# Optimization experiments

Measured on AMD Instinct MI355X. Metric: run time of the kernel, lower is better.

## Reference

```python
import jax, jax.numpy as jnp
import numpy as np

EPS = 1e-7  # tf.keras.backend.epsilon()

def setup_inputs() -> dict:
    key = jax.random.key(0)
    k1, k2, k3, k4 = jax.random.split(key, 4)
    B, S, D = 8, 2048, 768
    scale = 1.0 / np.sqrt(D)
    return {
        "x1": jax.random.normal(k1, (B, S, D), dtype=jnp.float32),
        "x2": jax.random.normal(k2, (B, S, D), dtype=jnp.float32),
        "Wq": jax.random.normal(k3, (D, D), dtype=jnp.float32) * scale,
        "bq": jnp.zeros((D,), dtype=jnp.float32),
        "Wk": jax.random.normal(k4, (D, D), dtype=jnp.float32) * scale,
        "bk": jnp.zeros((D,), dtype=jnp.float32),
    }

def reference(x1, x2, Wq, bq, Wk, bk):
    # q: [B,S1,D], k: [B,S2,D]
    q = jnp.einsum('bsd,de->bse', x1, Wq) + bq
    k = jnp.einsum('btd,de->bte', x2, Wk) + bk
    qk = jnp.einsum('bsd,btd->bst', q, k)          # [B,S1,S2]
    w = jnp.exp(jnp.tanh(qk))
    w = w / (jnp.sum(w, axis=1, keepdims=True) + EPS)  # normalize over S1
    return jnp.sum(w * qk, axis=1)                 # [B,S2]
```

## Files before the change

### kernel.cpp

```cpp
#include <hip/hip_runtime.h>
#include <hip/hip_bf16.h>

typedef __bf16 bf16_t;
typedef __bf16 bf16x8 __attribute__((ext_vector_type(8)));
typedef __bf16 bf16x4 __attribute__((ext_vector_type(4)));
typedef float  f32x4  __attribute__((ext_vector_type(4)));

#define D_DIM 768
#define S_DIM 2048
#define B_DIM 8
#define M_TOT (B_DIM * S_DIM)
#define BK 32
#define LDS_PAD 40

__global__ __launch_bounds__(256)
void transpose_weights(const float* __restrict__ Wq, const float* __restrict__ Wk,
                       bf16_t* __restrict__ Wqt, bf16_t* __restrict__ Wkt) {
    __shared__ float tile[32][33];
    const float* W  = blockIdx.z ? Wk  : Wq;
    bf16_t*      Wt = blockIdx.z ? Wkt : Wqt;
    int tx = threadIdx.x & 31, ty = threadIdx.x >> 5;
    int bx = blockIdx.x, by = blockIdx.y;
#pragma unroll
    for (int i = 0; i < 4; i++) {
        int k = bx * 32 + ty + i * 8;
        int n = by * 32 + tx;
        tile[ty + i * 8][tx] = W[k * D_DIM + n];
    }
    __syncthreads();
#pragma unroll
    for (int i = 0; i < 4; i++) {
        int n = by * 32 + ty + i * 8;
        int k = bx * 32 + tx;
        Wt[n * D_DIM + k] = (bf16_t)tile[tx][ty + i * 8];
    }
}

__global__ __launch_bounds__(256)
void proj_gemm(const float* __restrict__ X, const bf16_t* __restrict__ Wt,
               const float* __restrict__ bias, bf16_t* __restrict__ Out) {
    __shared__ bf16_t lds_a[128][LDS_PAD];
    __shared__ bf16_t lds_b[128][LDS_PAD];

    const int m0 = blockIdx.y * 128;
    const int n0 = blockIdx.x * 128;
    const int tid  = threadIdx.x;
    const int lane = tid & 63;
    const int wid  = tid >> 6;
    const int wm   = wid & 1;
    const int wn   = wid >> 1;
    const int lrow = lane & 15;
    const int quad = lane >> 4;

    f32x4 acc[4][4];
#pragma unroll
    for (int i = 0; i < 4; i++)
#pragma unroll
        for (int j = 0; j < 4; j++) acc[i][j] = (f32x4){0.f, 0.f, 0.f, 0.f};

    const int ar = tid >> 3, ac = tid & 7;
    const int br = tid >> 2, bc = tid & 3;

    for (int k0 = 0; k0 < D_DIM; k0 += BK) {
#pragma unroll
        for (int p = 0; p < 4; p++) {
            int row = ar + p * 32;
            const float4 v = *(const float4*)(X + (size_t)(m0 + row) * D_DIM + k0 + ac * 4);
            bf16x4 b;
            b[0] = (bf16_t)v.x; b[1] = (bf16_t)v.y; b[2] = (bf16_t)v.z; b[3] = (bf16_t)v.w;
            *(bf16x4*)&lds_a[row][ac * 4] = b;
        }
#pragma unroll
        for (int p = 0; p < 2; p++) {
            int row = br + p * 64;
            *(uint4*)&lds_b[row][bc * 8] =
                *(const uint4*)(Wt + (size_t)(n0 + row) * D_DIM + k0 + bc * 8);
        }
        __syncthreads();

        bf16x8 af[4], bfr[4];
#pragma unroll
        for (int f = 0; f < 4; f++) {
            af[f]  = *(const bf16x8*)&lds_a[wm * 64 + f * 16 + lrow][quad * 8];
            bfr[f] = *(const bf16x8*)&lds_b[wn * 64 + f * 16 + lrow][quad * 8];
        }
#pragma unroll
        for (int fm = 0; fm < 4; fm++)
#pragma unroll
            for (int fn = 0; fn < 4; fn++)
                acc[fm][fn] = __builtin_amdgcn_mfma_f32_16x16x32_bf16(
                    af[fm], bfr[fn], acc[fm][fn], 0, 0, 0);
        __syncthreads();
    }

#pragma unroll
    for (int fn = 0; fn < 4; fn++) {
        int col = n0 + wn * 64 + fn * 16 + lrow;
        float bv = bias[col];
#pragma unroll
        for (int fm = 0; fm < 4; fm++) {
            int rbase = m0 + wm * 64 + fm * 16 + quad * 4;
#pragma unroll
            for (int r = 0; r < 4; r++)
                Out[(size_t)(rbase + r) * D_DIM + col] = (bf16_t)(acc[fm][fn][r] + bv);
        }
    }
}

__global__ __launch_bounds__(256)
void attn_reduce(const bf16_t* __restrict__ Q, const bf16_t* __restrict__ K,
                 float* __restrict__ num, float* __restrict__ den) {
    __shared__ bf16_t lds_a[128][LDS_PAD];
    __shared__ bf16_t lds_b[128][LDS_PAD];
    __shared__ float red[2][2][128];

    const int b  = blockIdx.z;
    const int s0 = blockIdx.y * 128;
    const int t0 = blockIdx.x * 128;
    const bf16_t* Qb = Q + (size_t)b * S_DIM * D_DIM;
    const bf16_t* Kb = K + (size_t)b * S_DIM * D_DIM;

    const int tid  = threadIdx.x;
    const int lane = tid & 63;
    const int wid  = tid >> 6;
    const int wm   = wid & 1;
    const int wn   = wid >> 1;
    const int lrow = lane & 15;
    const int quad = lane >> 4;

    f32x4 acc[4][4];
#pragma unroll
    for (int i = 0; i < 4; i++)
#pragma unroll
        for (int j = 0; j < 4; j++) acc[i][j] = (f32x4){0.f, 0.f, 0.f, 0.f};

    const int br = tid >> 2, bc = tid & 3;

    for (int k0 = 0; k0 < D_DIM; k0 += BK) {
#pragma unroll
        for (int p = 0; p < 2; p++) {
            int row = br + p * 64;
            *(uint4*)&lds_a[row][bc * 8] =
                *(const uint4*)(Qb + (size_t)(s0 + row) * D_DIM + k0 + bc * 8);
            *(uint4*)&lds_b[row][bc * 8] =
                *(const uint4*)(Kb + (size_t)(t0 + row) * D_DIM + k0 + bc * 8);
        }
        __syncthreads();

        bf16x8 af[4], bfr[4];
#pragma unroll
        for (int f = 0; f < 4; f++) {
            af[f]  = *(const bf16x8*)&lds_a[wm * 64 + f * 16 + lrow][quad * 8];
            bfr[f] = *(const bf16x8*)&lds_b[wn * 64 + f * 16 + lrow][quad * 8];
        }
#pragma unroll
        for (int fm = 0; fm < 4; fm++)
#pragma unroll
            for (int fn = 0; fn < 4; fn++)
                acc[fm][fn] = __builtin_amdgcn_mfma_f32_16x16x32_bf16(
                    af[fm], bfr[fn], acc[fm][fn], 0, 0, 0);
        __syncthreads();
    }

    float sw[4], swv[4];
#pragma unroll
    for (int fn = 0; fn < 4; fn++) { sw[fn] = 0.f; swv[fn] = 0.f; }
#pragma unroll
    for (int fm = 0; fm < 4; fm++)
#pragma unroll
        for (int fn = 0; fn < 4; fn++)
#pragma unroll
            for (int r = 0; r < 4; r++) {
                float v = acc[fm][fn][r];
                float e2 = __expf(2.f * v);
                float t  = 1.f - 2.f / (e2 + 1.f);
                float w  = __expf(t);
                sw[fn]  += w;
                swv[fn] += w * v;
            }
#pragma unroll
    for (int fn = 0; fn < 4; fn++) {
        sw[fn]  += __shfl_xor(sw[fn], 16);  sw[fn]  += __shfl_xor(sw[fn], 32);
        swv[fn] += __shfl_xor(swv[fn], 16); swv[fn] += __shfl_xor(swv[fn], 32);
    }
    if (quad == 0) {
#pragma unroll
        for (int fn = 0; fn < 4; fn++) {
            red[0][wm][wn * 64 + fn * 16 + lrow] = sw[fn];
            red[1][wm][wn * 64 + fn * 16 + lrow] = swv[fn];
        }
    }
    __syncthreads();
    if (tid < 128) {
        int t = t0 + tid;
        atomicAdd(&den[b * S_DIM + t], red[0][0][tid] + red[0][1][tid]);
        atomicAdd(&num[b * S_DIM + t], red[1][0][tid] + red[1][1][tid]);
    }
}

__global__ __launch_bounds__(256)
void finalize(const float* __restrict__ num, const float* __restrict__ den,
              float* __restrict__ out, int n) {
    int i = blockIdx.x * 256 + threadIdx.x;
    if (i < n) out[i] = num[i] / (den[i] + 1e-7f);
}

extern "C" void kernel_launch(void* const* d_in, const int* in_sizes, int n_in,
                              void* d_out, int out_size, void* d_ws, size_t ws_size,
                              hipStream_t stream) {
    (void)in_sizes; (void)n_in; (void)out_size; (void)ws_size;
    const float* x1 = (const float*)d_in[0];
    const float* x2 = (const float*)d_in[1];
    const float* Wq = (const float*)d_in[2];
    const float* bq = (const float*)d_in[3];
    const float* Wk = (const float*)d_in[4];
    const float* bk = (const float*)d_in[5];
    float* out = (float*)d_out;

    char* ws = (char*)d_ws;
    size_t off = 0;
    bf16_t* qb  = (bf16_t*)(ws + off); off += (size_t)M_TOT * D_DIM * 2;
    bf16_t* kb  = (bf16_t*)(ws + off); off += (size_t)M_TOT * D_DIM * 2;
    bf16_t* Wqt = (bf16_t*)(ws + off); off += (size_t)D_DIM * D_DIM * 2;
    bf16_t* Wkt = (bf16_t*)(ws + off); off += (size_t)D_DIM * D_DIM * 2;
    float*  num = (float*)(ws + off);  off += (size_t)M_TOT * 4;
    float*  den = (float*)(ws + off);  off += (size_t)M_TOT * 4;

    hipMemsetAsync(num, 0, (size_t)M_TOT * 4 * 2, stream);

    transpose_weights<<<dim3(24, 24, 2), 256, 0, stream>>>(Wq, Wk, Wqt, Wkt);
    proj_gemm<<<dim3(6, 128), 256, 0, stream>>>(x1, Wqt, bq, qb);
    proj_gemm<<<dim3(6, 128), 256, 0, stream>>>(x2, Wkt, bk, kb);
    attn_reduce<<<dim3(16, 16, 8), 256, 0, stream>>>(qb, kb, num, den);
    finalize<<<dim3((M_TOT + 255) / 256), 256, 0, stream>>>(num, den, out, M_TOT);
}
```

Before: 300.4 us.

## Load GEMM tiles with global_load_lds and pre-cast inputs to bf16

Both GEMM kernels now stage tiles straight from global memory into LDS using the global_load_lds builtin, with an unpadded LDS layout, instead of routing them through registers. To make this possible for the projection, x1 and x2 are first converted to bf16 by a separate cast kernel. The two projection GEMMs are merged into one launch with a z dimension. The extra cast pass adds memory traffic and workspace, and removing the LDS padding may introduce bank conflicts on the fragment reads.

```diff
diff --git a/kernel.cpp b/kernel.cpp
--- a/kernel.cpp
+++ b/kernel.cpp
@@ -11,7 +11,24 @@
 #define B_DIM 8
 #define M_TOT (B_DIM * S_DIM)
 #define BK 32
-#define LDS_PAD 40
+
+#define GLOAD_LDS16(g, l) __builtin_amdgcn_global_load_lds( \
+    (const __attribute__((address_space(1))) unsigned int*)(g), \
+    (__attribute__((address_space(3))) unsigned int*)(l), 16, 0, 0)
+
+__global__ __launch_bounds__(256)
+void cast_inputs(const float* __restrict__ x1, const float* __restrict__ x2,
+                 bf16_t* __restrict__ o1, bf16_t* __restrict__ o2) {
+    const float* x = blockIdx.z ? x2 : x1;
+    bf16_t*      o = blockIdx.z ? o2 : o1;
+    size_t i = ((size_t)blockIdx.x * 256 + threadIdx.x) * 8;
+    float4 a = *(const float4*)(x + i);
+    float4 b = *(const float4*)(x + i + 4);
+    bf16x8 r;
+    r[0] = (bf16_t)a.x; r[1] = (bf16_t)a.y; r[2] = (bf16_t)a.z; r[3] = (bf16_t)a.w;
+    r[4] = (bf16_t)b.x; r[5] = (bf16_t)b.y; r[6] = (bf16_t)b.z; r[7] = (bf16_t)b.w;
+    *(bf16x8*)(o + i) = r;
+}
 
 __global__ __launch_bounds__(256)
 void transpose_weights(const float* __restrict__ Wq, const float* __restrict__ Wk,
@@ -37,10 +54,17 @@
 }
 
 __global__ __launch_bounds__(256)
-void proj_gemm(const float* __restrict__ X, const bf16_t* __restrict__ Wt,
-               const float* __restrict__ bias, bf16_t* __restrict__ Out) {
-    __shared__ bf16_t lds_a[128][LDS_PAD];
-    __shared__ bf16_t lds_b[128][LDS_PAD];
+void proj_gemm(const bf16_t* __restrict__ x1b, const bf16_t* __restrict__ x2b,
+               const bf16_t* __restrict__ Wqt, const bf16_t* __restrict__ Wkt,
+               const float* __restrict__ bq, const float* __restrict__ bk,
+               bf16_t* __restrict__ qb, bf16_t* __restrict__ kb) {
+    __shared__ bf16_t lds_a[128 * BK];
+    __shared__ bf16_t lds_b[128 * BK];
+
+    const bf16_t* X    = blockIdx.z ? x2b : x1b;
+    const bf16_t* Wt   = blockIdx.z ? Wkt : Wqt;
+    const float*  bias = blockIdx.z ? bk  : bq;
+    bf16_t*       Out  = blockIdx.z ? kb  : qb;
 
     const int m0 = blockIdx.y * 128;
     const int n0 = blockIdx.x * 128;
@@ -58,31 +82,25 @@
 #pragma unroll
         for (int j = 0; j < 4; j++) acc[i][j] = (f32x4){0.f, 0.f, 0.f, 0.f};
 
-    const int ar = tid >> 3, ac = tid & 7;
-    const int br = tid >> 2, bc = tid & 3;
+    const int srow = wid * 32 + (lane >> 2);
+    const int scol = (lane & 3) * 8;
+    const bf16_t* ag = X  + (size_t)(m0 + srow) * D_DIM + scol;
+    const bf16_t* bg = Wt + (size_t)(n0 + srow) * D_DIM + scol;
+    bf16_t* la = &lds_a[(wid * 32) * BK];
+    bf16_t* lb = &lds_b[(wid * 32) * BK];
 
     for (int k0 = 0; k0 < D_DIM; k0 += BK) {
-#pragma unroll
-        for (int p = 0; p < 4; p++) {
-            int row = ar + p * 32;
-            const float4 v = *(const float4*)(X + (size_t)(m0 + row) * D_DIM + k0 + ac * 4);
-            bf16x4 b;
-            b[0] = (bf16_t)v.x; b[1] = (bf16_t)v.y; b[2] = (bf16_t)v.z; b[3] = (bf16_t)v.w;
-            *(bf16x4*)&lds_a[row][ac * 4] = b;
-        }
-#pragma unroll
-        for (int p = 0; p < 2; p++) {
-            int row = br + p * 64;
-            *(uint4*)&lds_b[row][bc * 8] =
-                *(const uint4*)(Wt + (size_t)(n0 + row) * D_DIM + k0 + bc * 8);
-        }
+        GLOAD_LDS16(ag + k0,              la);
+        GLOAD_LDS16(ag + k0 + 16 * D_DIM, la + 16 * BK);
+        GLOAD_LDS16(bg + k0,              lb);
+        GLOAD_LDS16(bg + k0 + 16 * D_DIM, lb + 16 * BK);
         __syncthreads();
 
         bf16x8 af[4], bfr[4];
 #pragma unroll
         for (int f = 0; f < 4; f++) {
-            af[f]  = *(const bf16x8*)&lds_a[wm * 64 + f * 16 + lrow][quad * 8];
-            bfr[f] = *(const bf16x8*)&lds_b[wn * 64 + f * 16 + lrow][quad * 8];
+            af[f]  = *(const bf16x8*)&lds_a[(wm * 64 + f * 16 + lrow) * BK + quad * 8];
+            bfr[f] = *(const bf16x8*)&lds_b[(wn * 64 + f * 16 + lrow) * BK + quad * 8];
         }
 #pragma unroll
         for (int fm = 0; fm < 4; fm++)
@@ -110,8 +128,8 @@
 __global__ __launch_bounds__(256)
 void attn_reduce(const bf16_t* __restrict__ Q, const bf16_t* __restrict__ K,
                  float* __restrict__ num, float* __restrict__ den) {
-    __shared__ bf16_t lds_a[128][LDS_PAD];
-    __shared__ bf16_t lds_b[128][LDS_PAD];
+    __shared__ bf16_t lds_a[128 * BK];
+    __shared__ bf16_t lds_b[128 * BK];
     __shared__ float red[2][2][128];
 
     const int b  = blockIdx.z;
@@ -134,24 +152,25 @@
 #pragma unroll
         for (int j = 0; j < 4; j++) acc[i][j] = (f32x4){0.f, 0.f, 0.f, 0.f};
 
-    const int br = tid >> 2, bc = tid & 3;
+    const int srow = wid * 32 + (lane >> 2);
+    const int scol = (lane & 3) * 8;
+    const bf16_t* qg = Qb + (size_t)(s0 + srow) * D_DIM + scol;
+    const bf16_t* kg = Kb + (size_t)(t0 + srow) * D_DIM + scol;
+    bf16_t* la = &lds_a[(wid * 32) * BK];
+    bf16_t* lb = &lds_b[(wid * 32) * BK];
 
     for (int k0 = 0; k0 < D_DIM; k0 += BK) {
-#pragma unroll
-        for (int p = 0; p < 2; p++) {
-            int row = br + p * 64;
-            *(uint4*)&lds_a[row][bc * 8] =
-                *(const uint4*)(Qb + (size_t)(s0 + row) * D_DIM + k0 + bc * 8);
-            *(uint4*)&lds_b[row][bc * 8] =
-                *(const uint4*)(Kb + (size_t)(t0 + row) * D_DIM + k0 + bc * 8);
-        }
+        GLOAD_LDS16(qg + k0,              la);
+        GLOAD_LDS16(qg + k0 + 16 * D_DIM, la + 16 * BK);
+        GLOAD_LDS16(kg + k0,              lb);
+        GLOAD_LDS16(kg + k0 + 16 * D_DIM, lb + 16 * BK);
         __syncthreads();
 
         bf16x8 af[4], bfr[4];
 #pragma unroll
         for (int f = 0; f < 4; f++) {
-            af[f]  = *(const bf16x8*)&lds_a[wm * 64 + f * 16 + lrow][quad * 8];
-            bfr[f] = *(const bf16x8*)&lds_b[wn * 64 + f * 16 + lrow][quad * 8];
+            af[f]  = *(const bf16x8*)&lds_a[(wm * 64 + f * 16 + lrow) * BK + quad * 8];
+            bfr[f] = *(const bf16x8*)&lds_b[(wn * 64 + f * 16 + lrow) * BK + quad * 8];
         }
 #pragma unroll
         for (int fm = 0; fm < 4; fm++)
@@ -221,6 +240,8 @@
     size_t off = 0;
     bf16_t* qb  = (bf16_t*)(ws + off); off += (size_t)M_TOT * D_DIM * 2;
     bf16_t* kb  = (bf16_t*)(ws + off); off += (size_t)M_TOT * D_DIM * 2;
+    bf16_t* x1b = (bf16_t*)(ws + off); off += (size_t)M_TOT * D_DIM * 2;
+    bf16_t* x2b = (bf16_t*)(ws + off); off += (size_t)M_TOT * D_DIM * 2;
     bf16_t* Wqt = (bf16_t*)(ws + off); off += (size_t)D_DIM * D_DIM * 2;
     bf16_t* Wkt = (bf16_t*)(ws + off); off += (size_t)D_DIM * D_DIM * 2;
     float*  num = (float*)(ws + off);  off += (size_t)M_TOT * 4;
@@ -228,9 +249,9 @@
 
     hipMemsetAsync(num, 0, (size_t)M_TOT * 4 * 2, stream);
 
+    cast_inputs<<<dim3(6144, 1, 2), 256, 0, stream>>>(x1, x2, x1b, x2b);
     transpose_weights<<<dim3(24, 24, 2), 256, 0, stream>>>(Wq, Wk, Wqt, Wkt);
-    proj_gemm<<<dim3(6, 128), 256, 0, stream>>>(x1, Wqt, bq, qb);
-    proj_gemm<<<dim3(6, 128), 256, 0, stream>>>(x2, Wkt, bk, kb);
+    proj_gemm<<<dim3(6, 128, 2), 256, 0, stream>>>(x1b, x2b, Wqt, Wkt, bq, bk, qb, kb);
     attn_reduce<<<dim3(16, 16, 8), 256, 0, stream>>>(qb, kb, num, den);
     finalize<<<dim3((M_TOT + 255) / 256), 256, 0, stream>>>(num, den, out, M_TOT);
 }
```

After: 281.1 us. -6.4%, faster.

## Use direct global-to-LDS loads with XOR swizzle, BK=64, merged projection launch

Applied to the files above, without the earlier changes.

Replaces register-staged LDS fills with global_load_lds direct copies into an XOR-swizzled, unpadded LDS layout, and doubles the K tile to 64 so each loop iteration issues two MFMA k-steps per barrier pair. The two projection GEMMs are merged into one launch via blockIdx.z, and their output is staged through LDS so global stores are coalesced 16-byte writes. The aim is to cut LDS bank conflicts, VGPR traffic and barrier count. In exchange, LDS use per block grows to 32 KB, which may reduce occupancy, and there is still no double buffering.

```diff
diff --git a/kernel.cpp b/kernel.cpp
--- a/kernel.cpp
+++ b/kernel.cpp
@@ -3,15 +3,17 @@
 
 typedef __bf16 bf16_t;
 typedef __bf16 bf16x8 __attribute__((ext_vector_type(8)));
-typedef __bf16 bf16x4 __attribute__((ext_vector_type(4)));
 typedef float  f32x4  __attribute__((ext_vector_type(4)));
 
 #define D_DIM 768
 #define S_DIM 2048
 #define B_DIM 8
 #define M_TOT (B_DIM * S_DIM)
-#define BK 32
-#define LDS_PAD 40
+#define BK 64
+
+#define GLOAD_LDS16(g, l) __builtin_amdgcn_global_load_lds( \
+    (const __attribute__((address_space(1))) unsigned int*)(g), \
+    (__attribute__((address_space(3))) unsigned int*)(l), 16, 0, 0)
 
 __global__ __launch_bounds__(256)
 void transpose_weights(const float* __restrict__ Wq, const float* __restrict__ Wk,
@@ -37,10 +39,16 @@
 }
 
 __global__ __launch_bounds__(256)
-void proj_gemm(const float* __restrict__ X, const bf16_t* __restrict__ Wt,
-               const float* __restrict__ bias, bf16_t* __restrict__ Out) {
-    __shared__ bf16_t lds_a[128][LDS_PAD];
-    __shared__ bf16_t lds_b[128][LDS_PAD];
+void proj_gemm(const float* __restrict__ x1, const float* __restrict__ x2,
+               const bf16_t* __restrict__ Wqt, const bf16_t* __restrict__ Wkt,
+               const float* __restrict__ bq, const float* __restrict__ bk,
+               bf16_t* __restrict__ qb, bf16_t* __restrict__ kb) {
+    __shared__ bf16_t lds[2][128 * BK];
+
+    const float*  X    = blockIdx.z ? x2  : x1;
+    const bf16_t* Wt   = blockIdx.z ? Wkt : Wqt;
+    const float*  bias = blockIdx.z ? bk  : bq;
+    bf16_t*       Out  = blockIdx.z ? kb  : qb;
 
     const int m0 = blockIdx.y * 128;
     const int n0 = blockIdx.x * 128;
@@ -58,61 +66,80 @@
 #pragma unroll
         for (int j = 0; j < 4; j++) acc[i][j] = (f32x4){0.f, 0.f, 0.f, 0.f};
 
-    const int ar = tid >> 3, ac = tid & 7;
-    const int br = tid >> 2, bc = tid & 3;
+    const int arow  = tid >> 1;
+    const int ahalf = (tid & 1) * 4;
+    const float* agp = X + (size_t)(m0 + arow) * D_DIM + ahalf * 8;
+    bf16_t* alds = &lds[0][arow * BK];
+
+    const bf16_t* bgp = Wt + (size_t)n0 * D_DIM;
 
     for (int k0 = 0; k0 < D_DIM; k0 += BK) {
 #pragma unroll
-        for (int p = 0; p < 4; p++) {
-            int row = ar + p * 32;
-            const float4 v = *(const float4*)(X + (size_t)(m0 + row) * D_DIM + k0 + ac * 4);
-            bf16x4 b;
-            b[0] = (bf16_t)v.x; b[1] = (bf16_t)v.y; b[2] = (bf16_t)v.z; b[3] = (bf16_t)v.w;
-            *(bf16x4*)&lds_a[row][ac * 4] = b;
-        }
-#pragma unroll
-        for (int p = 0; p < 2; p++) {
-            int row = br + p * 64;
-            *(uint4*)&lds_b[row][bc * 8] =
-                *(const uint4*)(Wt + (size_t)(n0 + row) * D_DIM + k0 + bc * 8);
-        }
-        __syncthreads();
-
-        bf16x8 af[4], bfr[4];
-#pragma unroll
-        for (int f = 0; f < 4; f++) {
-            af[f]  = *(const bf16x8*)&lds_a[wm * 64 + f * 16 + lrow][quad * 8];
-            bfr[f] = *(const bf16x8*)&lds_b[wn * 64 + f * 16 + lrow][quad * 8];
-        }
-#pragma unroll
-        for (int fm = 0; fm < 4; fm++)
-#pragma unroll
-            for (int fn = 0; fn < 4; fn++)
-                acc[fm][fn] = __builtin_amdgcn_mfma_f32_16x16x32_bf16(
-                    af[fm], bfr[fn], acc[fm][fn], 0, 0, 0);
-        __syncthreads();
-    }
-
+        for (int i = 0; i < 4; i++) {
+            int linear = wid * 256 + i * 64 + lane;
+            int row  = linear >> 3;
+            int c    = (linear & 7) ^ (row & 7);
+            GLOAD_LDS16(bgp + (size_t)row * D_DIM + k0 + c * 8,
+                        &lds[1][(size_t)(wid * 256 + i * 64) * 8]);
+        }
+#pragma unroll
+        for (int c = 0; c < 4; c++) {
+            float4 u = *(const float4*)(agp + k0 + c * 8);
+            float4 v = *(const float4*)(agp + k0 + c * 8 + 4);
+            bf16x8 r;
+            r[0] = (bf16_t)u.x; r[1] = (bf16_t)u.y; r[2] = (bf16_t)u.z; r[3] = (bf16_t)u.w;
+            r[4] = (bf16_t)v.x; r[5] = (bf16_t)v.y; r[6] = (bf16_t)v.z; r[7] = (bf16_t)v.w;
+            *(bf16x8*)&alds[((ahalf + c) ^ (arow & 7)) * 8] = r;
+        }
+        __syncthreads();
+
+#pragma unroll
+        for (int j = 0; j < 2; j++) {
+            bf16x8 af[4], bfr[4];
+#pragma unroll
+            for (int f = 0; f < 4; f++) {
+                int ra = wm * 64 + f * 16 + lrow;
+                int rb = wn * 64 + f * 16 + lrow;
+                af[f]  = *(const bf16x8*)&lds[0][(ra * 8 + ((j * 4 + quad) ^ (ra & 7))) * 8];
+                bfr[f] = *(const bf16x8*)&lds[1][(rb * 8 + ((j * 4 + quad) ^ (rb & 7))) * 8];
+            }
+#pragma unroll
+            for (int fm = 0; fm < 4; fm++)
+#pragma unroll
+                for (int fn = 0; fn < 4; fn++)
+                    acc[fm][fn] = __builtin_amdgcn_mfma_f32_16x16x32_bf16(
+                        af[fm], bfr[fn], acc[fm][fn], 0, 0, 0);
+        }
+        __syncthreads();
+    }
+
+    bf16_t* cbuf = &lds[0][0];
 #pragma unroll
     for (int fn = 0; fn < 4; fn++) {
-        int col = n0 + wn * 64 + fn * 16 + lrow;
-        float bv = bias[col];
+        int col = wn * 64 + fn * 16 + lrow;
+        float bv = bias[n0 + col];
 #pragma unroll
         for (int fm = 0; fm < 4; fm++) {
-            int rbase = m0 + wm * 64 + fm * 16 + quad * 4;
+            int rbase = wm * 64 + fm * 16 + quad * 4;
 #pragma unroll
             for (int r = 0; r < 4; r++)
-                Out[(size_t)(rbase + r) * D_DIM + col] = (bf16_t)(acc[fm][fn][r] + bv);
-        }
+                cbuf[(rbase + r) * 128 + col] = (bf16_t)(acc[fm][fn][r] + bv);
+        }
+    }
+    __syncthreads();
+    {
+        int row = tid >> 1, cb = (tid & 1) * 64;
+#pragma unroll
+        for (int i = 0; i < 8; i++)
+            *(uint4*)(Out + (size_t)(m0 + row) * D_DIM + n0 + cb + i * 8) =
+                *(const uint4*)&cbuf[row * 128 + cb + i * 8];
     }
 }
 
 __global__ __launch_bounds__(256)
 void attn_reduce(const bf16_t* __restrict__ Q, const bf16_t* __restrict__ K,
                  float* __restrict__ num, float* __restrict__ den) {
-    __shared__ bf16_t lds_a[128][LDS_PAD];
-    __shared__ bf16_t lds_b[128][LDS_PAD];
-    __shared__ float red[2][2][128];
+    __shared__ bf16_t lds[2][128 * BK];
 
     const int b  = blockIdx.z;
     const int s0 = blockIdx.y * 128;
@@ -134,31 +161,36 @@
 #pragma unroll
         for (int j = 0; j < 4; j++) acc[i][j] = (f32x4){0.f, 0.f, 0.f, 0.f};
 
-    const int br = tid >> 2, bc = tid & 3;
-
     for (int k0 = 0; k0 < D_DIM; k0 += BK) {
 #pragma unroll
-        for (int p = 0; p < 2; p++) {
-            int row = br + p * 64;
-            *(uint4*)&lds_a[row][bc * 8] =
-                *(const uint4*)(Qb + (size_t)(s0 + row) * D_DIM + k0 + bc * 8);
-            *(uint4*)&lds_b[row][bc * 8] =
-                *(const uint4*)(Kb + (size_t)(t0 + row) * D_DIM + k0 + bc * 8);
-        }
-        __syncthreads();
-
-        bf16x8 af[4], bfr[4];
-#pragma unroll
-        for (int f = 0; f < 4; f++) {
-            af[f]  = *(const bf16x8*)&lds_a[wm * 64 + f * 16 + lrow][quad * 8];
-            bfr[f] = *(const bf16x8*)&lds_b[wn * 64 + f * 16 + lrow][quad * 8];
-        }
-#pragma unroll
-        for (int fm = 0; fm < 4; fm++)
-#pragma unroll
-            for (int fn = 0; fn < 4; fn++)
-                acc[fm][fn] = __builtin_amdgcn_mfma_f32_16x16x32_bf16(
-                    af[fm], bfr[fn], acc[fm][fn], 0, 0, 0);
+        for (int i = 0; i < 4; i++) {
+            int linear = wid * 256 + i * 64 + lane;
+            int row  = linear >> 3;
+            int c    = (linear & 7) ^ (row & 7);
+            GLOAD_LDS16(Qb + (size_t)(s0 + row) * D_DIM + k0 + c * 8,
+                        &lds[0][(size_t)(wid * 256 + i * 64) * 8]);
+            GLOAD_LDS16(Kb + (size_t)(t0 + row) * D_DIM + k0 + c * 8,
+                        &lds[1][(size_t)(wid * 256 + i * 64) * 8]);
+        }
+        __syncthreads();
+
+#pragma unroll
+        for (int j = 0; j < 2; j++) {
+            bf16x8 af[4], bfr[4];
+#pragma unroll
+            for (int f = 0; f < 4; f++) {
+                int ra = wm * 64 + f * 16 + lrow;
+                int rb = wn * 64 + f * 16 + lrow;
+                af[f]  = *(const bf16x8*)&lds[0][(ra * 8 + ((j * 4 + quad) ^ (ra & 7))) * 8];
+                bfr[f] = *(const bf16x8*)&lds[1][(rb * 8 + ((j * 4 + quad) ^ (rb & 7))) * 8];
+            }
+#pragma unroll
+            for (int fm = 0; fm < 4; fm++)
+#pragma unroll
+                for (int fn = 0; fn < 4; fn++)
+                    acc[fm][fn] = __builtin_amdgcn_mfma_f32_16x16x32_bf16(
+                        af[fm], bfr[fn], acc[fm][fn], 0, 0, 0);
+        }
         __syncthreads();
     }
 
@@ -183,18 +215,19 @@
         sw[fn]  += __shfl_xor(sw[fn], 16);  sw[fn]  += __shfl_xor(sw[fn], 32);
         swv[fn] += __shfl_xor(swv[fn], 16); swv[fn] += __shfl_xor(swv[fn], 32);
     }
+    float* red = (float*)&lds[0][0];
     if (quad == 0) {
 #pragma unroll
         for (int fn = 0; fn < 4; fn++) {
-            red[0][wm][wn * 64 + fn * 16 + lrow] = sw[fn];
-            red[1][wm][wn * 64 + fn * 16 + lrow] = swv[fn];
+            red[(0 * 2 + wm) * 128 + wn * 64 + fn * 16 + lrow] = sw[fn];
+            red[(1 * 2 + wm) * 128 + wn * 64 + fn * 16 + lrow] = swv[fn];
         }
     }
     __syncthreads();
     if (tid < 128) {
         int t = t0 + tid;
-        atomicAdd(&den[b * S_DIM + t], red[0][0][tid] + red[0][1][tid]);
-        atomicAdd(&num[b * S_DIM + t], red[1][0][tid] + red[1][1][tid]);
+        atomicAdd(&den[b * S_DIM + t], red[  0 + tid] + red[128 + tid]);
+        atomicAdd(&num[b * S_DIM + t], red[256 + tid] + red[384 + tid]);
     }
 }
 
@@ -229,8 +262,7 @@
     hipMemsetAsync(num, 0, (size_t)M_TOT * 4 * 2, stream);
 
     transpose_weights<<<dim3(24, 24, 2), 256, 0, stream>>>(Wq, Wk, Wqt, Wkt);
-    proj_gemm<<<dim3(6, 128), 256, 0, stream>>>(x1, Wqt, bq, qb);
-    proj_gemm<<<dim3(6, 128), 256, 0, stream>>>(x2, Wkt, bk, kb);
+    proj_gemm<<<dim3(6, 128, 2), 256, 0, stream>>>(x1, x2, Wqt, Wkt, bq, bk, qb, kb);
     attn_reduce<<<dim3(16, 16, 8), 256, 0, stream>>>(qb, kb, num, den);
     finalize<<<dim3((M_TOT + 255) / 256), 256, 0, stream>>>(num, den, out, M_TOT);
 }
```

Result: slower. 318.5 us (+6.0%).
